# Kernel tuning notes

Measured on AMD Instinct MI355X. Metric: run time of the kernel, lower is better.

Reference implementation:

```python
import jax, jax.numpy as jnp
import numpy as np

# GDN (gated delta-rule) linear attention, prefill path, single packed sequence,
# no initial conv/ssm state.
NUM_K_HEADS = 16
NUM_V_HEADS = 32
HEAD_K_DIM = 128
HEAD_V_DIM = 128
HIDDEN = 2048
CONV_K = 4
EPS = 1e-6
K_TOTAL = NUM_K_HEADS * HEAD_K_DIM
V_TOTAL = NUM_V_HEADS * HEAD_V_DIM
QKV_TOTAL = 2 * K_TOTAL + V_TOTAL


def setup_inputs() -> dict:
    key = jax.random.key(0)
    ks = jax.random.split(key, 9)
    T = 2048
    s = 0.02
    return {
        "hidden_states": jax.random.normal(ks[0], (T, HIDDEN), jnp.float32),
        "in_proj_qkv_weight": s * jax.random.normal(ks[1], (QKV_TOTAL, HIDDEN), jnp.float32),
        "in_proj_z_weight": s * jax.random.normal(ks[2], (V_TOTAL, HIDDEN), jnp.float32),
        "in_proj_a_weight": s * jax.random.normal(ks[3], (NUM_V_HEADS, HIDDEN), jnp.float32),
        "in_proj_b_weight": s * jax.random.normal(ks[4], (NUM_V_HEADS, HIDDEN), jnp.float32),
        "conv1d_weight": 0.1 * jax.random.normal(ks[5], (QKV_TOTAL, CONV_K), jnp.float32),
        "out_proj_weight": s * jax.random.normal(ks[6], (HIDDEN, V_TOTAL), jnp.float32),
        "norm_weight": jnp.ones((HEAD_V_DIM,), jnp.float32),
        "A_log": jnp.log(jnp.linspace(1.0, 8.0, NUM_V_HEADS, dtype=jnp.float32)),
        "dt_bias": 0.5 * jax.random.normal(ks[7], (NUM_V_HEADS,), jnp.float32),
    }


def _causal_conv1d_silu(x, w):
    # x: [T, C], w: [C, K] depthwise causal conv + SiLU
    T = x.shape[0]
    K = w.shape[1]
    xp = jnp.pad(x, ((K - 1, 0), (0, 0)))
    y = xp[0:T] * w[:, 0]
    for j in range(1, K):  # small fixed K
        y = y + xp[j:j + T] * w[:, j]
    return jax.nn.silu(y)


def _l2norm(x):
    return x / jnp.sqrt(jnp.sum(x * x, axis=-1, keepdims=True) + EPS)


def _gdn_recurrence(q, k, v, g, beta, scale):
    # q,k: [T,Hv,Dk] (l2-normed, repeated over GQA groups), v: [T,Hv,Dv]
    # g,beta: [T,Hv]. State S: [Hv,Dk,Dv]. Gated delta rule:
    #   S <- exp(g)*S ; S <- S + k^T beta (v - k S) ; o = scale * q S
    Hv, Dk = q.shape[1], q.shape[2]
    Dv = v.shape[2]

    def step(S, inp):
        q_t, k_t, v_t, g_t, b_t = inp
        S = S * jnp.exp(g_t)[:, None, None]
        pred = jnp.einsum('hk,hkv->hv', k_t, S)
        delta = b_t[:, None] * (v_t - pred)
        S = S + jnp.einsum('hk,hv->hkv', k_t, delta)
        o = jnp.einsum('hk,hkv->hv', q_t * scale, S)
        return S, o

    S0 = jnp.zeros((Hv, Dk, Dv), q.dtype)
    _, o = jax.lax.scan(step, S0, (q, k, v, g, beta))
    return o  # [T,Hv,Dv]


def reference(hidden_states, in_proj_qkv_weight, in_proj_z_weight, in_proj_a_weight,
              in_proj_b_weight, conv1d_weight, out_proj_weight, norm_weight, A_log, dt_bias):
    T = hidden_states.shape[0]
    mixed = hidden_states @ in_proj_qkv_weight.T            # [T, QKV_TOTAL]
    z = hidden_states @ in_proj_z_weight.T                  # [T, V_TOTAL]
    a = hidden_states @ in_proj_a_weight.T                  # [T, Hv]
    b = hidden_states @ in_proj_b_weight.T                  # [T, Hv]

    mixed = _causal_conv1d_silu(mixed, conv1d_weight)

    q, k, v = jnp.split(mixed, [K_TOTAL, 2 * K_TOTAL], axis=-1)
    q = q.reshape(T, NUM_K_HEADS, HEAD_K_DIM)
    k = k.reshape(T, NUM_K_HEADS, HEAD_K_DIM)
    v = v.reshape(T, NUM_V_HEADS, HEAD_V_DIM)

    # qk l2-norm in kernel, GQA repeat to v heads
    q = _l2norm(q)
    k = _l2norm(k)
    ratio = NUM_V_HEADS // NUM_K_HEADS
    q = jnp.repeat(q, ratio, axis=1)
    k = jnp.repeat(k, ratio, axis=1)

    # fused_gdn_gating: g = -exp(A_log) * softplus(a + dt_bias); beta = sigmoid(b)
    g = -jnp.exp(A_log) * jax.nn.softplus(a + dt_bias)      # [T,Hv]
    beta = jax.nn.sigmoid(b)                                # [T,Hv]

    o = _gdn_recurrence(q, k, v, g, beta, HEAD_K_DIM ** -0.5)  # [T,Hv,Dv]

    # gated RMSNorm: rmsnorm(o) * norm_weight * silu(z)
    o = o * jax.lax.rsqrt(jnp.mean(o * o, axis=-1, keepdims=True) + EPS) * norm_weight
    o = o * jax.nn.silu(z.reshape(T, NUM_V_HEADS, HEAD_V_DIM))

    return o.reshape(T, -1) @ out_proj_weight.T             # [T, HIDDEN]
```

## Files before the change

kernel.cpp:

```cpp
#include <hip/hip_runtime.h>
#include <math.h>

#define T_SEQ     2048
#define HIDDEN_D  2048
#define NUM_KH    16
#define NUM_VH    32
#define HEAD_DIM  128
#define K_TOTAL   2048
#define V_TOTAL   4096
#define QKV_TOTAL 8192
#define EPS_F     1e-6f
#define CC        32
#define NCHUNK    (T_SEQ / CC)
#define NV        8

typedef __attribute__((ext_vector_type(4))) float f32x4;
typedef __attribute__((ext_vector_type(8))) short s16x8;
typedef __attribute__((ext_vector_type(8))) unsigned short u16x8;

__device__ __forceinline__ unsigned short f2bf(float f) {
    unsigned int u = __float_as_uint(f);
    u += 0x7FFFu + ((u >> 16) & 1u);
    return (unsigned short)(u >> 16);
}

__device__ __forceinline__ float bf2f(unsigned short h) {
    return __uint_as_float((unsigned int)h << 16);
}

__global__ __launch_bounds__(256) void cast_bf16_kernel(
    const float* __restrict__ src, unsigned short* __restrict__ dst, int n4)
{
    int idx = blockIdx.x * 256 + threadIdx.x;
    if (idx >= n4) return;
    float4 v = ((const float4*)src)[idx];
    ushort4 o;
    o.x = f2bf(v.x); o.y = f2bf(v.y); o.z = f2bf(v.z); o.w = f2bf(v.w);
    ((ushort4*)dst)[idx] = o;
}

__global__ __launch_bounds__(256) void gemm_bt_bf16(
    const unsigned short* __restrict__ A, const unsigned short* __restrict__ B,
    float* __restrict__ C, int M, int N, int K)
{
    __shared__ unsigned short As[128 * 64];
    __shared__ unsigned short Bs[128 * 64];
    const int tid  = threadIdx.x;
    const int wave = tid >> 6;
    const int lane = tid & 63;
    const int m0 = blockIdx.y * 128;
    const int n0 = blockIdx.x * 128;
    const int wm = (wave >> 1) * 64;
    const int wn = (wave & 1) * 64;

    f32x4 acc[4][4];
    f32x4 zero = {0.f, 0.f, 0.f, 0.f};
#pragma unroll
    for (int i = 0; i < 4; ++i)
#pragma unroll
        for (int j = 0; j < 4; ++j) acc[i][j] = zero;

    const int srow = lane >> 3;
    const int scol = (lane & 7) * 8;
    const int rm = lane & 15;
    const int koq = (lane >> 4) * 8;

    for (int kt = 0; kt < K; kt += 64) {
#pragma unroll
        for (int l = 0; l < 4; ++l) {
            const int r0 = wave * 32 + l * 8;
            const unsigned short* ga =
                A + (size_t)(m0 + r0 + srow) * K + kt + scol;
            const unsigned short* gb =
                B + (size_t)(n0 + r0 + srow) * K + kt + scol;
            __builtin_amdgcn_global_load_lds(
                (const __attribute__((address_space(1))) void*)ga,
                (__attribute__((address_space(3))) void*)&As[r0 * 64], 16, 0, 0);
            __builtin_amdgcn_global_load_lds(
                (const __attribute__((address_space(1))) void*)gb,
                (__attribute__((address_space(3))) void*)&Bs[r0 * 64], 16, 0, 0);
        }
        __syncthreads();

#pragma unroll
        for (int ks = 0; ks < 2; ++ks) {
            const int ko = ks * 32 + koq;
            s16x8 af[4], bfr[4];
#pragma unroll
            for (int i = 0; i < 4; ++i) {
                af[i]  = *(const s16x8*)&As[(wm + i * 16 + rm) * 64 + ko];
                bfr[i] = *(const s16x8*)&Bs[(wn + i * 16 + rm) * 64 + ko];
            }
#pragma unroll
            for (int i = 0; i < 4; ++i)
#pragma unroll
                for (int j = 0; j < 4; ++j)
                    acc[i][j] = __builtin_amdgcn_mfma_f32_16x16x32_bf16(
                        af[i], bfr[j], acc[i][j], 0, 0, 0);
        }
        __syncthreads();
    }

    const int cr = (lane >> 4) * 4;
    const int ccol = lane & 15;
#pragma unroll
    for (int i = 0; i < 4; ++i)
#pragma unroll
        for (int j = 0; j < 4; ++j) {
#pragma unroll
            for (int r = 0; r < 4; ++r)
                C[(size_t)(m0 + wm + i * 16 + cr + r) * N
                  + n0 + wn + j * 16 + ccol] = acc[i][j][r];
        }
}

__global__ __launch_bounds__(256) void gemm_nt_64(
    const float* __restrict__ A, const float* __restrict__ B,
    float* __restrict__ C, int M, int N, int K)
{
    __shared__ float As[16][68];
    __shared__ float Bs[16][68];
    const int tid = threadIdx.x;
    const int m0 = blockIdx.y * 64;
    const int n0 = blockIdx.x * 64;
    const int tm = tid >> 4;
    const int tn = tid & 15;
    const int lr = tid >> 2;
    const int lc = (tid & 3) * 4;

    float acc[4][4];
#pragma unroll
    for (int i = 0; i < 4; ++i)
#pragma unroll
        for (int j = 0; j < 4; ++j) acc[i][j] = 0.f;

    for (int kt = 0; kt < K; kt += 16) {
        float4 av = *(const float4*)(A + (size_t)(m0 + lr) * K + kt + lc);
        float4 bv = *(const float4*)(B + (size_t)(n0 + lr) * K + kt + lc);
        As[lc + 0][lr] = av.x; As[lc + 1][lr] = av.y;
        As[lc + 2][lr] = av.z; As[lc + 3][lr] = av.w;
        Bs[lc + 0][lr] = bv.x; Bs[lc + 1][lr] = bv.y;
        Bs[lc + 2][lr] = bv.z; Bs[lc + 3][lr] = bv.w;
        __syncthreads();
#pragma unroll
        for (int kk = 0; kk < 16; ++kk) {
            float4 a4 = *(const float4*)&As[kk][tm * 4];
            float4 b4 = *(const float4*)&Bs[kk][tn * 4];
            float a[4] = {a4.x, a4.y, a4.z, a4.w};
            float b[4] = {b4.x, b4.y, b4.z, b4.w};
#pragma unroll
            for (int i = 0; i < 4; ++i)
#pragma unroll
                for (int j = 0; j < 4; ++j)
                    acc[i][j] = fmaf(a[i], b[j], acc[i][j]);
        }
        __syncthreads();
    }
#pragma unroll
    for (int i = 0; i < 4; ++i) {
        float4 o = make_float4(acc[i][0], acc[i][1], acc[i][2], acc[i][3]);
        *(float4*)(C + (size_t)(m0 + tm * 4 + i) * N + n0 + tn * 4) = o;
    }
}

__global__ __launch_bounds__(256) void concat_ab_kernel(
    const float* __restrict__ Wa, const float* __restrict__ Wb,
    float* __restrict__ Wab)
{
    int idx = blockIdx.x * 256 + threadIdx.x;
    int half = 16384;
    const float* src = (idx < half) ? Wa : Wb;
    int off = (idx < half) ? idx : idx - half;
    ((float4*)Wab)[idx] = ((const float4*)src)[off];
}

__global__ __launch_bounds__(256) void gating_finalize_kernel(
    const float* __restrict__ ab, const float* __restrict__ A_log,
    const float* __restrict__ dt_bias, float* __restrict__ g,
    float* __restrict__ beta)
{
    int idx = blockIdx.x * 256 + threadIdx.x;
    int t = idx >> 5, h = idx & 31;
    float a = ab[t * 64 + h] + dt_bias[h];
    float b = ab[t * 64 + 32 + h];
    float sp = (a > 20.f) ? a : log1pf(expf(a));
    g[idx] = -expf(A_log[h]) * sp;
    beta[idx] = 1.f / (1.f + expf(-b));
}

__global__ __launch_bounds__(256) void conv_v_kernel(
    const float* __restrict__ mixed, const float* __restrict__ cw,
    float* __restrict__ vb)
{
    int idx = blockIdx.x * 256 + threadIdx.x;
    int c = idx & (V_TOTAL - 1);
    int t = idx >> 12;
    int ch = 2 * K_TOTAL + c;
    const float4 w = *(const float4*)(cw + (size_t)ch * 4);
    const float* base = mixed + (size_t)t * QKV_TOTAL + ch;
    float y = w.w * base[0];
    if (t >= 1) y = fmaf(w.z, base[-QKV_TOTAL], y);
    if (t >= 2) y = fmaf(w.y, base[-2 * QKV_TOTAL], y);
    if (t >= 3) y = fmaf(w.x, base[-3 * QKV_TOTAL], y);
    vb[idx] = y / (1.f + expf(-y));
}

__global__ __launch_bounds__(64) void convqk_l2_kernel(
    const float* __restrict__ mixed, const float* __restrict__ cw,
    unsigned short* __restrict__ qk_bf)
{
    const int row = blockIdx.x;
    const int t = row >> 5;
    const int r = row & 31;
    const int lane = threadIdx.x;
    const int c = r * HEAD_DIM + lane * 2;
    const float4 w0 = *(const float4*)(cw + (size_t)c * 4);
    const float4 w1 = *(const float4*)(cw + (size_t)(c + 1) * 4);
    const float* base = mixed + (size_t)t * QKV_TOTAL + c;
    float2 x0 = *(const float2*)base;
    float y0 = w0.w * x0.x, y1 = w1.w * x0.y;
    if (t >= 1) {
        float2 x = *(const float2*)(base - QKV_TOTAL);
        y0 = fmaf(w0.z, x.x, y0); y1 = fmaf(w1.z, x.y, y1);
    }
    if (t >= 2) {
        float2 x = *(const float2*)(base - 2 * QKV_TOTAL);
        y0 = fmaf(w0.y, x.x, y0); y1 = fmaf(w1.y, x.y, y1);
    }
    if (t >= 3) {
        float2 x = *(const float2*)(base - 3 * QKV_TOTAL);
        y0 = fmaf(w0.x, x.x, y0); y1 = fmaf(w1.x, x.y, y1);
    }
    y0 = y0 / (1.f + expf(-y0));
    y1 = y1 / (1.f + expf(-y1));
    float s = y0 * y0 + y1 * y1;
    for (int off = 32; off > 0; off >>= 1) s += __shfl_down(s, off);
    s = __shfl(s, 0);
    float inv = rsqrtf(s + EPS_F);
    unsigned short* qb = qk_bf + (size_t)t * 4096 + c;
    qb[0] = f2bf(y0 * inv);
    qb[1] = f2bf(y1 * inv);
}

__global__ __launch_bounds__(256) void gdn_p1(
    const unsigned short* __restrict__ qk_bf, const float* __restrict__ g,
    const float* __restrict__ beta, unsigned short* __restrict__ PTbuf,
    unsigned short* __restrict__ K2buf, float* __restrict__ lam_g,
    float* __restrict__ bet_g)
{
    __shared__ float Kn[CC][132];
    __shared__ float Qn[CC][132];
    __shared__ float Wm[CC][33];
    __shared__ float Tld[CC][36];
    __shared__ float Pm[CC][33];
    __shared__ float Trl[CC][33];
    __shared__ float cums[CC];
    __shared__ float betas[CC];
    __shared__ float rlS[CC];

    const int tid = threadIdx.x;
    const int h   = blockIdx.x;
    const int cix = blockIdx.y;
    const int t0  = cix * CC;
    const int kh  = h >> 1;
    const float scale = 0.08838834764831845f;
    const size_t mb = ((size_t)cix * NUM_VH + h);
    const size_t sb = mb * CC;

    if (tid < CC) {
        float x = g[(size_t)(t0 + tid) * NUM_VH + h];
        float bv = beta[(size_t)(t0 + tid) * NUM_VH + h];
#pragma unroll
        for (int off = 1; off < 32; off <<= 1) {
            float n = __shfl_up(x, off);
            if (tid >= off) x += n;
        }
        cums[tid] = x;
        betas[tid] = bv;
        float c31 = __shfl(x, 31);
        lam_g[sb + tid] = expf(x);
        bet_g[sb + tid] = bv;
        rlS[tid] = expf(c31 - x);
    }
#pragma unroll
    for (int p = 0; p < 2; ++p) {
        int idx = p * 256 + tid;
        int i = idx >> 4, ch = (idx & 15) * 8;
        const unsigned short* qr =
            qk_bf + (size_t)(t0 + i) * 4096 + kh * HEAD_DIM + ch;
        u16x8 q8 = *(const u16x8*)qr;
        u16x8 k8 = *(const u16x8*)(qr + K_TOTAL);
        float4 kf0, kf1, qf0, qf1;
        kf0.x = bf2f(k8[0]); kf0.y = bf2f(k8[1]);
        kf0.z = bf2f(k8[2]); kf0.w = bf2f(k8[3]);
        kf1.x = bf2f(k8[4]); kf1.y = bf2f(k8[5]);
        kf1.z = bf2f(k8[6]); kf1.w = bf2f(k8[7]);
        qf0.x = bf2f(q8[0]) * scale; qf0.y = bf2f(q8[1]) * scale;
        qf0.z = bf2f(q8[2]) * scale; qf0.w = bf2f(q8[3]) * scale;
        qf1.x = bf2f(q8[4]) * scale; qf1.y = bf2f(q8[5]) * scale;
        qf1.z = bf2f(q8[6]) * scale; qf1.w = bf2f(q8[7]) * scale;
        *(float4*)&Kn[i][ch]     = kf0;
        *(float4*)&Kn[i][ch + 4] = kf1;
        *(float4*)&Qn[i][ch]     = qf0;
        *(float4*)&Qn[i][ch + 4] = qf1;
    }
    __syncthreads();

    {
        const int i0 = (tid >> 4) * 2, j0 = (tid & 15) * 2;
        float wa[2][2] = {{0.f, 0.f}, {0.f, 0.f}};
        float pa[2][2] = {{0.f, 0.f}, {0.f, 0.f}};
        for (int k = 0; k < HEAD_DIM; k += 4) {
            float4 a0 = *(const float4*)&Kn[i0][k];
            float4 a1 = *(const float4*)&Kn[i0 + 1][k];
            float4 b0 = *(const float4*)&Kn[j0][k];
            float4 b1 = *(const float4*)&Kn[j0 + 1][k];
            float4 c0 = *(const float4*)&Qn[i0][k];
            float4 c1 = *(const float4*)&Qn[i0 + 1][k];
            const float* ap0 = (const float*)&a0;
            const float* ap1 = (const float*)&a1;
            const float* bp0 = (const float*)&b0;
            const float* bp1 = (const float*)&b1;
            const float* cp0 = (const float*)&c0;
            const float* cp1 = (const float*)&c1;
#pragma unroll
            for (int cc = 0; cc < 4; ++cc) {
                wa[0][0] = fmaf(ap0[cc], bp0[cc], wa[0][0]);
                wa[0][1] = fmaf(ap0[cc], bp1[cc], wa[0][1]);
                wa[1][0] = fmaf(ap1[cc], bp0[cc], wa[1][0]);
                wa[1][1] = fmaf(ap1[cc], bp1[cc], wa[1][1]);
                pa[0][0] = fmaf(cp0[cc], bp0[cc], pa[0][0]);
                pa[0][1] = fmaf(cp0[cc], bp1[cc], pa[0][1]);
                pa[1][0] = fmaf(cp1[cc], bp0[cc], pa[1][0]);
                pa[1][1] = fmaf(cp1[cc], bp1[cc], pa[1][1]);
            }
        }
#pragma unroll
        for (int di = 0; di < 2; ++di)
#pragma unroll
            for (int dj = 0; dj < 2; ++dj) {
                int i = i0 + di, j = j0 + dj;
                float rr = expf(fminf(cums[i] - cums[j], 0.f));
                Wm[i][j] = (j < i) ? betas[i] * rr * wa[di][dj] : 0.f;
                Pm[i][j] = (j <= i) ? rr * pa[di][dj] : 0.f;
            }
    }
    __syncthreads();

    {
        const int col = tid >> 3, tk = tid & 7;
        if (tk == 0) Tld[0][col] = (col == 0) ? 1.f : 0.f;
        for (int i = 1; i < CC; ++i) {
            float part = 0.f;
            for (int j = tk; j < i; j += 8)
                part = fmaf(Wm[i][j], Tld[j][col], part);
            part += __shfl_xor(part, 4);
            part += __shfl_xor(part, 2);
            part += __shfl_xor(part, 1);
            if (tk == 0) Tld[i][col] = ((i == col) ? 1.f : 0.f) - part;
        }
    }
    __syncthreads();

    {
        const int i = tid >> 3, j0 = (tid & 7) * 4;
        const float r = rlS[i];
#pragma unroll
        for (int e = 0; e < 4; ++e)
            Trl[i][j0 + e] = Tld[i][j0 + e] * r;
        float4 accp = {0.f, 0.f, 0.f, 0.f};
        for (int m = 0; m < CC; ++m) {
            float pv = Pm[i][m];
            float4 tv = *(const float4*)&Tld[m][j0];
            accp.x = fmaf(pv, tv.x, accp.x);
            accp.y = fmaf(pv, tv.y, accp.y);
            accp.z = fmaf(pv, tv.z, accp.z);
            accp.w = fmaf(pv, tv.w, accp.w);
        }
        ushort4 pt4;
        pt4.x = f2bf(accp.x); pt4.y = f2bf(accp.y);
        pt4.z = f2bf(accp.z); pt4.w = f2bf(accp.w);
        *(ushort4*)(PTbuf + mb * (CC * CC) + tid * 4) = pt4;
    }
    __syncthreads();

    {
        const int m0 = tid >> 3;
        const int q  = (tid & 7) * 4;
        float acc[4][4];
#pragma unroll
        for (int c = 0; c < 4; ++c)
#pragma unroll
            for (int e = 0; e < 4; ++e) acc[c][e] = 0.f;
        for (int j = 0; j < CC; ++j) {
            float t = Trl[j][m0];
#pragma unroll
            for (int c = 0; c < 4; ++c) {
                float4 a = *(const float4*)&Kn[j][q + 32 * c];
                acc[c][0] = fmaf(t, a.x, acc[c][0]);
                acc[c][1] = fmaf(t, a.y, acc[c][1]);
                acc[c][2] = fmaf(t, a.z, acc[c][2]);
                acc[c][3] = fmaf(t, a.w, acc[c][3]);
            }
        }
        unsigned short* kout =
            K2buf + mb * (CC * HEAD_DIM) + m0 * HEAD_DIM + q;
#pragma unroll
        for (int c = 0; c < 4; ++c) {
            ushort4 o4;
            o4.x = f2bf(acc[c][0]); o4.y = f2bf(acc[c][1]);
            o4.z = f2bf(acc[c][2]); o4.w = f2bf(acc[c][3]);
            *(ushort4*)(kout + 32 * c) = o4;
        }
    }
}

__global__ __launch_bounds__(256, 2) void gdn_p2(
    const float* __restrict__ vb, const unsigned short* __restrict__ qk_bf,
    const unsigned short* __restrict__ PTbuf,
    const unsigned short* __restrict__ K2buf, const float* __restrict__ lam_g,
    const float* __restrict__ bet_g, float* __restrict__ o)
{
    __shared__ unsigned short Kn[CC][128];
    __shared__ unsigned short Qn[CC][128];
    __shared__ unsigned short K2l[2][CC][128];
    __shared__ float PTl[2][CC][36];
    __shared__ float Sm[HEAD_DIM][NV + 2];
    __shared__ float Dl[CC][NV + 2];
    __shared__ float lamS[2][CC], betS[2][CC];

    const int tid = threadIdx.x;
    const int wv  = tid >> 6;
    const int ln  = tid & 63;
    const int h   = blockIdx.x >> 4;
    const int V0  = (blockIdx.x & 15) * NV;
    const int kh  = h >> 1;
    const float scale = 0.08838834764831845f;

    const int ri = tid >> 3;
    const int rn = (tid & 3) * 2;
    const int hh = (tid >> 2) & 1;
    const int rx2 = ri & 3;

    const int fk = (tid >> 3) * 4;
    const int sn = tid & 7;

    const int drow = ln >> 4;
    const int dc   = ln & 15;

#define DMA_KQ(T0)                                                            \
    {                                                                         \
        _Pragma("unroll")                                                     \
        for (int p = 0; p < 2; ++p) {                                         \
            const int i = p * 16 + wv * 4 + drow;                             \
            const int sc = 2 * ((dc >> 1) ^ (i & 3)) + (dc & 1);              \
            const unsigned short* sq = qk_bf + (size_t)((T0) + i) * 4096      \
                                       + kh * HEAD_DIM + sc * 8;              \
            __builtin_amdgcn_global_load_lds(                                 \
                (const __attribute__((address_space(1))) void*)(sq + K_TOTAL),\
                (__attribute__((address_space(3))) void*)                     \
                    &Kn[p * 16 + wv * 4][0], 16, 0, 0);                       \
            __builtin_amdgcn_global_load_lds(                                 \
                (const __attribute__((address_space(1))) void*)sq,            \
                (__attribute__((address_space(3))) void*)                     \
                    &Qn[p * 16 + wv * 4][0], 16, 0, 0);                       \
        }                                                                     \
    }

#define DMA_K2(MB, BUF)                                                       \
    {                                                                         \
        _Pragma("unroll")                                                     \
        for (int p = 0; p < 2; ++p) {                                         \
            const unsigned short* sk = K2buf + (MB) * (CC * HEAD_DIM)         \
                                       + p * 2048 + wv * 512 + ln * 8;        \
            __builtin_amdgcn_global_load_lds(                                 \
                (const __attribute__((address_space(1))) void*)sk,            \
                (__attribute__((address_space(3))) void*)                     \
                    &K2l[BUF][p * 16 + wv * 4][0], 16, 0, 0);                 \
        }                                                                     \
    }

#pragma unroll
    for (int c = 0; c < 4; ++c) Sm[fk + c][sn] = 0.f;

    DMA_KQ(0);
    DMA_K2((size_t)h, 0);
    {
        ushort4 pt0 = *(const ushort4*)(PTbuf + (size_t)h * (CC * CC) + tid * 4);
        float4 pf;
        pf.x = bf2f(pt0.x); pf.y = bf2f(pt0.y);
        pf.z = bf2f(pt0.z); pf.w = bf2f(pt0.w);
        *(float4*)&PTl[0][tid >> 3][(tid & 7) * 4] = pf;
        if (tid < CC) {
            lamS[0][tid] = lam_g[(size_t)h * CC + tid];
            betS[0][tid] = bet_g[(size_t)h * CC + tid];
        }
    }
    float2 vR = *(const float2*)(vb + (size_t)ri * V_TOTAL
                                 + h * HEAD_DIM + V0 + rn);

    int cur = 0;
    for (int cix = 0; cix < NCHUNK; ++cix) {
        const int t0 = cix * CC;
        __syncthreads();

        const float lam = lamS[cur][ri];
        const float bet = betS[cur][ri];
        float r1x = 0.f, r1y = 0.f, r2x = 0.f, r2y = 0.f;
#pragma unroll
        for (int kk = 0; kk < 8; ++kk) {
            const int pc = (2 * (kk ^ rx2) + hh) * 8;
            const int cl = kk * 16 + hh * 8;
            u16x8 kv = *(const u16x8*)&Kn[ri][pc];
            u16x8 qv = *(const u16x8*)&Qn[ri][pc];
#pragma unroll
            for (int c8 = 0; c8 < 8; ++c8) {
                float kf = bf2f(kv[c8]);
                float qf = bf2f(qv[c8]);
                float2 s = *(const float2*)&Sm[cl + c8][rn];
                r1x = fmaf(kf, s.x, r1x);
                r1y = fmaf(kf, s.y, r1y);
                r2x = fmaf(qf, s.x, r2x);
                r2y = fmaf(qf, s.y, r2y);
            }
        }
        r1x += __shfl_xor(r1x, 4);
        r1y += __shfl_xor(r1y, 4);
        r2x += __shfl_xor(r2x, 4);
        r2y += __shfl_xor(r2y, 4);
        {
            float dlx = bet * (vR.x - lam * r1x);
            float dly = bet * (vR.y - lam * r1y);
            if (hh == 0) { Dl[ri][rn] = dlx; Dl[ri][rn + 1] = dly; }
        }
        const float lsc = lam * scale;
        float ox = r2x * lsc, oy = r2y * lsc;
        __syncthreads();

        const int nxt = cur ^ 1;
        ushort4 ptN; float lamN = 0.f, betN = 0.f; float2 vN;
        const int more = (cix + 1 < NCHUNK);
        if (more) {
            const int t0n = t0 + CC;
            const size_t mbn = (size_t)(cix + 1) * NUM_VH + h;
            DMA_KQ(t0n);
            DMA_K2(mbn, nxt);
            ptN = *(const ushort4*)(PTbuf + mbn * (CC * CC) + tid * 4);
            if (tid < CC) {
                lamN = lam_g[mbn * CC + tid];
                betN = bet_g[mbn * CC + tid];
            }
            vN = *(const float2*)(vb + (size_t)(t0n + ri) * V_TOTAL
                                  + h * HEAD_DIM + V0 + rn);
        }

        {
            for (int j = 0; j < CC; ++j) {
                float p = PTl[cur][ri][j];
                float2 d = *(const float2*)&Dl[j][rn];
                ox = fmaf(p, d.x, ox);
                oy = fmaf(p, d.y, oy);
            }
            if (hh == 0)
                *(float2*)(o + (size_t)(t0 + ri) * V_TOTAL + h * HEAD_DIM + V0 + rn)
                    = make_float2(ox, oy);
        }

        {
            const float lamL = lamS[cur][CC - 1];
            float s0 = lamL * Sm[fk + 0][sn];
            float s1 = lamL * Sm[fk + 1][sn];
            float s2 = lamL * Sm[fk + 2][sn];
            float s3 = lamL * Sm[fk + 3][sn];
            for (int j = 0; j < CC; ++j) {
                ushort4 kk = *(const ushort4*)&K2l[cur][j][fk];
                float d = Dl[j][sn];
                s0 = fmaf(bf2f(kk.x), d, s0);
                s1 = fmaf(bf2f(kk.y), d, s1);
                s2 = fmaf(bf2f(kk.z), d, s2);
                s3 = fmaf(bf2f(kk.w), d, s3);
            }
            Sm[fk + 0][sn] = s0;
            Sm[fk + 1][sn] = s1;
            Sm[fk + 2][sn] = s2;
            Sm[fk + 3][sn] = s3;
        }

        if (more) {
            float4 pf;
            pf.x = bf2f(ptN.x); pf.y = bf2f(ptN.y);
            pf.z = bf2f(ptN.z); pf.w = bf2f(ptN.w);
            *(float4*)&PTl[nxt][tid >> 3][(tid & 7) * 4] = pf;
            if (tid < CC) { lamS[nxt][tid] = lamN; betS[nxt][tid] = betN; }
            vR = vN;
        }
        cur = nxt;
    }
#undef DMA_KQ
#undef DMA_K2
}

__global__ __launch_bounds__(64) void rmsnorm_gate_kernel(
    float* __restrict__ o, const float* __restrict__ z,
    const float* __restrict__ nw)
{
    const int row = blockIdx.x;
    float* p = o + (size_t)row * HEAD_DIM;
    const float* zp = z + (size_t)row * HEAD_DIM;
    const int lane = threadIdx.x;
    float2 v = *(float2*)(p + lane * 2);
    float s = v.x * v.x + v.y * v.y;
    for (int off = 32; off > 0; off >>= 1) s += __shfl_down(s, off);
    s = __shfl(s, 0);
    float inv = rsqrtf(s * (1.f / HEAD_DIM) + EPS_F);
    float2 zv = *(float2*)(zp + lane * 2);
    float2 wv = *(const float2*)(nw + lane * 2);
    v.x = v.x * inv * wv.x * (zv.x / (1.f + expf(-zv.x)));
    v.y = v.y * inv * wv.y * (zv.y / (1.f + expf(-zv.y)));
    *(float2*)(p + lane * 2) = v;
}

extern "C" void kernel_launch(void* const* d_in, const int* in_sizes, int n_in,
                              void* d_out, int out_size, void* d_ws,
                              size_t ws_size, hipStream_t stream)
{
    const float* hs    = (const float*)d_in[0];
    const float* Wqkv  = (const float*)d_in[1];
    const float* Wz    = (const float*)d_in[2];
    const float* Wa    = (const float*)d_in[3];
    const float* Wb    = (const float*)d_in[4];
    const float* cw    = (const float*)d_in[5];
    const float* Wout  = (const float*)d_in[6];
    const float* nw    = (const float*)d_in[7];
    const float* A_log = (const float*)d_in[8];
    const float* dtb   = (const float*)d_in[9];
    float* out = (float*)d_out;

    float* F     = (float*)d_ws;
    float* mixed = F;
    float* ob    = F;
    unsigned short* PTbuf = (unsigned short*)(F + (size_t)8388608);
    unsigned short* K2buf = (unsigned short*)(F + (size_t)9437184);
    float* lam_b = F + (size_t)13631488;
    float* bet_b = F + (size_t)13697024;
    unsigned short* hs_bf   = (unsigned short*)(F + (size_t)16777216);
    unsigned short* Wqkv_bf = (unsigned short*)(F + (size_t)18874368);
    float* vb = F + (size_t)16777216;
    unsigned short* qk_bf = (unsigned short*)(F + (size_t)25165824);
    unsigned short* Wz_bf   = (unsigned short*)(F + (size_t)27262976);
    float* Wab = F + (size_t)27262976;
    float* ab  = F + (size_t)27394048;
    float* zb  = F + (size_t)33554432;
    unsigned short* ob_bf   = (unsigned short*)(F + (size_t)33554432);
    unsigned short* Wout_bf = (unsigned short*)(F + (size_t)37748736);
    float* gb = F + (size_t)41943040;
    float* bb = F + (size_t)42008576;

    cast_bf16_kernel<<<1048576 / 256, 256, 0, stream>>>(hs, hs_bf, 1048576);
    cast_bf16_kernel<<<4194304 / 256, 256, 0, stream>>>(Wqkv, Wqkv_bf, 4194304);
    cast_bf16_kernel<<<2097152 / 256, 256, 0, stream>>>(Wz, Wz_bf, 2097152);
    gemm_bt_bf16<<<dim3(QKV_TOTAL / 128, T_SEQ / 128), 256, 0, stream>>>(
        hs_bf, Wqkv_bf, mixed, T_SEQ, QKV_TOTAL, HIDDEN_D);
    gemm_bt_bf16<<<dim3(V_TOTAL / 128, T_SEQ / 128), 256, 0, stream>>>(
        hs_bf, Wz_bf, zb, T_SEQ, V_TOTAL, HIDDEN_D);
    concat_ab_kernel<<<32768 / 256, 256, 0, stream>>>(Wa, Wb, Wab);
    gemm_nt_64<<<dim3(1, T_SEQ / 64), 256, 0, stream>>>(
        hs, Wab, ab, T_SEQ, 64, HIDDEN_D);
    gating_finalize_kernel<<<(T_SEQ * NUM_VH) / 256, 256, 0, stream>>>(
        ab, A_log, dtb, gb, bb);
    conv_v_kernel<<<(T_SEQ * V_TOTAL) / 256, 256, 0, stream>>>(
        mixed, cw, vb);
    convqk_l2_kernel<<<T_SEQ * 32, 64, 0, stream>>>(mixed, cw, qk_bf);
    gdn_p1<<<dim3(NUM_VH, NCHUNK), 256, 0, stream>>>(
        qk_bf, gb, bb, PTbuf, K2buf, lam_b, bet_b);
    gdn_p2<<<NUM_VH * (HEAD_DIM / NV), 256, 0, stream>>>(
        vb, qk_bf, PTbuf, K2buf, lam_b, bet_b, ob);
    rmsnorm_gate_kernel<<<T_SEQ * NUM_VH, 64, 0, stream>>>(ob, zb, nw);
    cast_bf16_kernel<<<2097152 / 256, 256, 0, stream>>>(ob, ob_bf, 2097152);
    cast_bf16_kernel<<<2097152 / 256, 256, 0, stream>>>(Wout, Wout_bf, 2097152);
    gemm_bt_bf16<<<dim3(HIDDEN_D / 128, T_SEQ / 128), 256, 0, stream>>>(
        ob_bf, Wout_bf, out, T_SEQ, HIDDEN_D, V_TOTAL);
}
```

Before: 929.4 us.

## Fuse input casts, fold bf16 cast into rmsnorm, swizzle GEMM block order

```diff
diff --git a/kernel.cpp b/kernel.cpp
--- a/kernel.cpp
+++ b/kernel.cpp
@@ -39,6 +39,22 @@
     ((ushort4*)dst)[idx] = o;
 }
 
+__global__ __launch_bounds__(256) void cast3_kernel(
+    const float* __restrict__ hs, const float* __restrict__ Wqkv,
+    const float* __restrict__ Wz, unsigned short* __restrict__ hs_bf,
+    unsigned short* __restrict__ Wqkv_bf, unsigned short* __restrict__ Wz_bf)
+{
+    int idx = blockIdx.x * 256 + threadIdx.x;
+    const float* src; unsigned short* dst; int off;
+    if (idx < 1048576)      { src = hs;   dst = hs_bf;   off = idx; }
+    else if (idx < 5242880) { src = Wqkv; dst = Wqkv_bf; off = idx - 1048576; }
+    else                    { src = Wz;   dst = Wz_bf;   off = idx - 5242880; }
+    float4 v = ((const float4*)src)[off];
+    ushort4 o;
+    o.x = f2bf(v.x); o.y = f2bf(v.y); o.z = f2bf(v.z); o.w = f2bf(v.w);
+    ((ushort4*)dst)[off] = o;
+}
+
 __global__ __launch_bounds__(256) void gemm_bt_bf16(
     const unsigned short* __restrict__ A, const unsigned short* __restrict__ B,
     float* __restrict__ C, int M, int N, int K)
@@ -48,8 +64,15 @@
     const int tid  = threadIdx.x;
     const int wave = tid >> 6;
     const int lane = tid & 63;
-    const int m0 = blockIdx.y * 128;
-    const int n0 = blockIdx.x * 128;
+
+    const int nx  = N >> 7;
+    const int nwg = nx * (M >> 7);
+    const int bid = blockIdx.y * nx + blockIdx.x;
+    const int cpx = nwg >> 3;
+    const int swz = (bid & 7) * cpx + (bid >> 3);
+    const int m0 = (swz / nx) * 128;
+    const int n0 = (swz % nx) * 128;
+
     const int wm = (wave >> 1) * 64;
     const int wn = (wave & 1) * 64;
 
@@ -601,23 +624,25 @@
 }
 
 __global__ __launch_bounds__(64) void rmsnorm_gate_kernel(
-    float* __restrict__ o, const float* __restrict__ z,
-    const float* __restrict__ nw)
+    const float* __restrict__ o, const float* __restrict__ z,
+    const float* __restrict__ nw, unsigned short* __restrict__ ob_bf)
 {
     const int row = blockIdx.x;
-    float* p = o + (size_t)row * HEAD_DIM;
+    const float* p = o + (size_t)row * HEAD_DIM;
     const float* zp = z + (size_t)row * HEAD_DIM;
     const int lane = threadIdx.x;
-    float2 v = *(float2*)(p + lane * 2);
+    float2 v = *(const float2*)(p + lane * 2);
     float s = v.x * v.x + v.y * v.y;
     for (int off = 32; off > 0; off >>= 1) s += __shfl_down(s, off);
     s = __shfl(s, 0);
     float inv = rsqrtf(s * (1.f / HEAD_DIM) + EPS_F);
-    float2 zv = *(float2*)(zp + lane * 2);
+    float2 zv = *(const float2*)(zp + lane * 2);
     float2 wv = *(const float2*)(nw + lane * 2);
     v.x = v.x * inv * wv.x * (zv.x / (1.f + expf(-zv.x)));
     v.y = v.y * inv * wv.y * (zv.y / (1.f + expf(-zv.y)));
-    *(float2*)(p + lane * 2) = v;
+    unsigned short* q = ob_bf + (size_t)row * HEAD_DIM + lane * 2;
+    q[0] = f2bf(v.x);
+    q[1] = f2bf(v.y);
 }
 
 extern "C" void kernel_launch(void* const* d_in, const int* in_sizes, int n_in,
@@ -640,6 +665,7 @@
     float* mixed = F;
     float* ob    = F;
     unsigned short* PTbuf = (unsigned short*)(F + (size_t)8388608);
+    unsigned short* ob_bf = (unsigned short*)(F + (size_t)8388608);
     unsigned short* K2buf = (unsigned short*)(F + (size_t)9437184);
     float* lam_b = F + (size_t)13631488;
     float* bet_b = F + (size_t)13697024;
@@ -651,14 +677,12 @@
     float* Wab = F + (size_t)27262976;
     float* ab  = F + (size_t)27394048;
     float* zb  = F + (size_t)33554432;
-    unsigned short* ob_bf   = (unsigned short*)(F + (size_t)33554432);
     unsigned short* Wout_bf = (unsigned short*)(F + (size_t)37748736);
     float* gb = F + (size_t)41943040;
     float* bb = F + (size_t)42008576;
 
-    cast_bf16_kernel<<<1048576 / 256, 256, 0, stream>>>(hs, hs_bf, 1048576);
-    cast_bf16_kernel<<<4194304 / 256, 256, 0, stream>>>(Wqkv, Wqkv_bf, 4194304);
-    cast_bf16_kernel<<<2097152 / 256, 256, 0, stream>>>(Wz, Wz_bf, 2097152);
+    cast3_kernel<<<7340032 / 256, 256, 0, stream>>>(
+        hs, Wqkv, Wz, hs_bf, Wqkv_bf, Wz_bf);
     gemm_bt_bf16<<<dim3(QKV_TOTAL / 128, T_SEQ / 128), 256, 0, stream>>>(
         hs_bf, Wqkv_bf, mixed, T_SEQ, QKV_TOTAL, HIDDEN_D);
     gemm_bt_bf16<<<dim3(V_TOTAL / 128, T_SEQ / 128), 256, 0, stream>>>(
@@ -675,8 +699,7 @@
         qk_bf, gb, bb, PTbuf, K2buf, lam_b, bet_b);
     gdn_p2<<<NUM_VH * (HEAD_DIM / NV), 256, 0, stream>>>(
         vb, qk_bf, PTbuf, K2buf, lam_b, bet_b, ob);
-    rmsnorm_gate_kernel<<<T_SEQ * NUM_VH, 64, 0, stream>>>(ob, zb, nw);
-    cast_bf16_kernel<<<2097152 / 256, 256, 0, stream>>>(ob, ob_bf, 2097152);
+    rmsnorm_gate_kernel<<<T_SEQ * NUM_VH, 64, 0, stream>>>(ob, zb, nw, ob_bf);
     cast_bf16_kernel<<<2097152 / 256, 256, 0, stream>>>(Wout, Wout_bf, 2097152);
     gemm_bt_bf16<<<dim3(HIDDEN_D / 128, T_SEQ / 128), 256, 0, stream>>>(
         ob_bf, Wout_bf, out, T_SEQ, HIDDEN_D, V_TOTAL);
```

Result: no change. 919.2 us (-1.1%).
